# Kernel tuning notes

Measured on AMD Instinct MI355X. Metric: run time of the kernel, lower is better.

## Reference

```python
import jax, jax.numpy as jnp
import numpy as np

N_HEADS = 32
N_KV_HEADS = 8
HEAD_DIM = 128
DIM = 4096
BATCH = 2
SEQ = 2048


def rope_freqs(seqlen, head_dim, theta=10000.0):
    inv_freq = 1.0 / (theta ** (np.arange(0, head_dim, 2, dtype=np.float32) / head_dim))
    t = np.arange(seqlen, dtype=np.float32)
    ang = np.outer(t, inv_freq)  # [S, head_dim//2]
    return jnp.asarray(np.cos(ang)), jnp.asarray(np.sin(ang))


def setup_inputs() -> dict:
    key = jax.random.key(0)
    ks = jax.random.split(key, 5)
    x = jax.random.normal(ks[0], (BATCH, SEQ, DIM), dtype=jnp.float32)
    wq = jax.random.normal(ks[1], (N_HEADS * HEAD_DIM, DIM), dtype=jnp.float32) * 0.02
    wk = jax.random.normal(ks[2], (N_KV_HEADS * HEAD_DIM, DIM), dtype=jnp.float32) * 0.02
    wv = jax.random.normal(ks[3], (N_KV_HEADS * HEAD_DIM, DIM), dtype=jnp.float32) * 0.02
    wo = jax.random.normal(ks[4], (DIM, N_HEADS * HEAD_DIM), dtype=jnp.float32) * 0.02
    freqs_cos, freqs_sin = rope_freqs(SEQ, HEAD_DIM)
    return {"x": x, "freqs_cos": freqs_cos, "freqs_sin": freqs_sin,
            "wq": wq, "wk": wk, "wv": wv, "wo": wo}


def apply_rope(x, cos, sin):
    # x: [B, S, H, D]; complex multiply on consecutive pairs (even=real, odd=imag)
    xf = x.astype(jnp.float32).reshape(*x.shape[:-1], HEAD_DIM // 2, 2)
    x0, x1 = xf[..., 0], xf[..., 1]
    c = cos[None, :, None, :]  # [1, S, 1, D/2]
    s = sin[None, :, None, :]
    o0 = x0 * c - x1 * s
    o1 = x0 * s + x1 * c
    return jnp.stack([o0, o1], axis=-1).reshape(x.shape).astype(x.dtype)


def reference(x, freqs_cos, freqs_sin, wq, wk, wv, wo):
    b, s, _ = x.shape
    g = N_HEADS // N_KV_HEADS  # GQA group size
    xq = (x @ wq.T).reshape(b, s, N_HEADS, HEAD_DIM)
    xk = (x @ wk.T).reshape(b, s, N_KV_HEADS, HEAD_DIM)
    xv = (x @ wv.T).reshape(b, s, N_KV_HEADS, HEAD_DIM)
    xq = apply_rope(xq, freqs_cos, freqs_sin)
    xk = apply_rope(xk, freqs_cos, freqs_sin)
    # GQA: group query heads per kv head without repeating k/v
    q = xq.reshape(b, s, N_KV_HEADS, g, HEAD_DIM)
    scale = 1.0 / jnp.sqrt(jnp.asarray(HEAD_DIM, dtype=x.dtype))
    scores = jnp.einsum("bqkgd,bskd->bkgqs", q, xk) * scale  # [B, KV, G, S, S]
    causal = jnp.tril(jnp.ones((s, s), dtype=bool))
    scores = jnp.where(causal, scores, jnp.asarray(-jnp.inf, dtype=scores.dtype))
    probs = jax.nn.softmax(scores, axis=-1)
    out = jnp.einsum("bkgqs,bskd->bqkgd", probs, xv).reshape(b, s, N_HEADS * HEAD_DIM)
    return out @ wo.T
```

## Files before the change

### kernel.cpp

```cpp
#include <hip/hip_runtime.h>
#include <hip/hip_bf16.h>

typedef short short8_t __attribute__((ext_vector_type(8)));
typedef float float4_t __attribute__((ext_vector_type(4)));

#define MFMA16(A, B, C) __builtin_amdgcn_mfma_f32_16x16x32_bf16((A), (B), (C), 0, 0, 0)

#define SEQ 2048
#define HD 128
#define NH 32
#define NKV 8

__device__ inline short f2bs(float f) {
    union { __hip_bfloat16 h; short s; } u;
    u.h = __float2bfloat16(f);
    return u.s;
}

__device__ inline short8_t load8(const __hip_bfloat16* p) {
    return *(const short8_t*)p;
}
__device__ inline short8_t load8(const float* p) {
    float4_t a = *(const float4_t*)p;
    float4_t b = *(const float4_t*)(p + 4);
    short8_t r;
    r[0] = f2bs(a[0]); r[1] = f2bs(a[1]); r[2] = f2bs(a[2]); r[3] = f2bs(a[3]);
    r[4] = f2bs(b[0]); r[5] = f2bs(b[1]); r[6] = f2bs(b[2]); r[7] = f2bs(b[3]);
    return r;
}

__device__ inline void store_c(__hip_bfloat16* p, float v) { *p = __float2bfloat16(v); }
__device__ inline void store_c(float* p, float v)          { *p = v; }

__device__ __forceinline__ void gld_lds16(const __hip_bfloat16* g, __hip_bfloat16* l) {
    __builtin_amdgcn_global_load_lds(
        (const __attribute__((address_space(1))) unsigned int*)g,
        (__attribute__((address_space(3))) unsigned int*)l,
        16, 0, 0);
}

__global__ __launch_bounds__(256) void cvt_bf16(
    const float* __restrict__ in, __hip_bfloat16* __restrict__ out, int n8)
{
    int stride = gridDim.x * 256;
    for (int i = blockIdx.x * 256 + threadIdx.x; i < n8; i += stride) {
        short8_t r = load8(in + (size_t)i * 8);
        *(short8_t*)(out + (size_t)i * 8) = r;
    }
}

template <typename TC, bool TRC = false>
__global__ __launch_bounds__(256) void gemm_bt(
    const __hip_bfloat16* __restrict__ A,
    const __hip_bfloat16* __restrict__ B,
    TC* __restrict__ C,
    int M, int N, int K)
{
    __shared__ __hip_bfloat16 As[128 * 32];
    __shared__ __hip_bfloat16 Bs[128 * 32];

    const int tid  = threadIdx.x;
    const int wave = tid >> 6;
    const int lane = tid & 63;
    const int quad = lane >> 4;
    const int l16  = lane & 15;
    const int m0 = blockIdx.y * 128;
    const int n0 = blockIdx.x * 128;
    const int wm = (wave >> 1) * 64;
    const int wn = (wave & 1) * 64;

    const int row0 = tid >> 2;
    const int col0 = (tid & 3) * 8;

    const __hip_bfloat16* Abase = A + (size_t)m0 * K;
    const __hip_bfloat16* Bbase = B + (size_t)n0 * K;
    __hip_bfloat16* AsW = As + wave * 512;
    __hip_bfloat16* BsW = Bs + wave * 512;

    float4_t acc[4][4] = {};

    for (int k0 = 0; k0 < K; k0 += 32) {
        __syncthreads();
        gld_lds16(Abase + (size_t)row0        * K + k0 + col0, AsW);
        gld_lds16(Abase + (size_t)(row0 + 64) * K + k0 + col0, AsW + 2048);
        gld_lds16(Bbase + (size_t)row0        * K + k0 + col0, BsW);
        gld_lds16(Bbase + (size_t)(row0 + 64) * K + k0 + col0, BsW + 2048);
        __syncthreads();

        short8_t af[4], bf[4];
#pragma unroll
        for (int t = 0; t < 4; t++)
            af[t] = *(const short8_t*)&As[(wm + t * 16 + l16) * 32 + quad * 8];
#pragma unroll
        for (int t = 0; t < 4; t++)
            bf[t] = *(const short8_t*)&Bs[(wn + t * 16 + l16) * 32 + quad * 8];
#pragma unroll
        for (int mt = 0; mt < 4; mt++)
#pragma unroll
            for (int nt = 0; nt < 4; nt++)
                acc[mt][nt] = MFMA16(af[mt], bf[nt], acc[mt][nt]);
    }

#pragma unroll
    for (int mt = 0; mt < 4; mt++)
#pragma unroll
        for (int nt = 0; nt < 4; nt++)
#pragma unroll
            for (int r = 0; r < 4; r++) {
                int row = m0 + wm + mt * 16 + quad * 4 + r;
                int col = n0 + wn + nt * 16 + l16;
                if constexpr (TRC) {
                    int bb = row >> 11, ss = row & (SEQ - 1);
                    C[((size_t)bb * N + col) * SEQ + ss] = __float2bfloat16(acc[mt][nt][r]);
                } else {
                    store_c(&C[(size_t)row * N + col], acc[mt][nt][r]);
                }
            }
}

template <typename TC>
__global__ __launch_bounds__(512, 2) void gemm256(
    const __hip_bfloat16* __restrict__ A,
    const __hip_bfloat16* __restrict__ B,
    TC* __restrict__ C,
    int M, int N, int K)
{
    __shared__ __hip_bfloat16 lds[65536];
    __hip_bfloat16* ldsA0 = lds;
    __hip_bfloat16* ldsB0 = lds + 16384;
    __hip_bfloat16* ldsA1 = lds + 32768;
    __hip_bfloat16* ldsB1 = lds + 49152;

    const int tid  = threadIdx.x;
    const int wave = tid >> 6;
    const int lane = tid & 63;
    const int quad = lane >> 4;
    const int l16  = lane & 15;
    const int wm = wave >> 2;
    const int wn = wave & 3;
    const int m0 = blockIdx.y * 256;
    const int n0 = blockIdx.x * 256;

    const __hip_bfloat16* Abase = A + (size_t)m0 * K;
    const __hip_bfloat16* Bbase = B + (size_t)n0 * K;

    float4_t acc[8][4] = {};
    short8_t af[4][2], bf[2][2];

#define FENCE  asm volatile("" ::: "memory")
#define BAR    { FENCE; __builtin_amdgcn_s_barrier(); FENCE; }
#define LGKM0  { asm volatile("s_waitcnt lgkmcnt(0)" ::: "memory");          \
                 __builtin_amdgcn_sched_barrier(0); }
#define LGKM8  asm volatile("s_waitcnt lgkmcnt(8)" ::: "memory")
#define VM4    asm volatile("s_waitcnt vmcnt(4)" ::: "memory")
#define VM0    asm volatile("s_waitcnt vmcnt(0)" ::: "memory")

#define STAGE(GBASE, LTILE, T, H)                                            \
    {                                                                        \
        _Pragma("unroll")                                                    \
        for (int j = 0; j < 2; j++) {                                        \
            int c = j * 512 + tid;                                           \
            int r = c >> 3, s = c & 7;                                       \
            gld_lds16((GBASE) + (size_t)((H) * 128 + r) * K + (T) * 64 +     \
                          ((s ^ (r & 7)) * 8),                               \
                      (LTILE) + (H) * 8192 + j * 4096 + wave * 512);         \
        }                                                                    \
    }

#define LDA_(QM, ABASE)                                                      \
    {                                                                        \
        _Pragma("unroll")                                                    \
        for (int mt = 0; mt < 4; mt++)                                       \
            _Pragma("unroll")                                                \
            for (int kk = 0; kk < 2; kk++) {                                 \
                int row = (QM) * 128 + wm * 64 + mt * 16 + l16;              \
                int sc  = (kk * 4 + quad) ^ (row & 7);                       \
                af[mt][kk] = *(const short8_t*)&(ABASE)[row * 64 + sc * 8];  \
            }                                                                \
    }

#define LDB_(QN, BBASE)                                                      \
    {                                                                        \
        _Pragma("unroll")                                                    \
        for (int nt = 0; nt < 2; nt++)                                       \
            _Pragma("unroll")                                                \
            for (int kk = 0; kk < 2; kk++) {                                 \
                int row = (QN) * 128 + wn * 32 + nt * 16 + l16;              \
                int sc  = (kk * 4 + quad) ^ (row & 7);                       \
                bf[nt][kk] = *(const short8_t*)&(BBASE)[row * 64 + sc * 8];  \
            }                                                                \
    }

#define QMM(QM, QN)                                                          \
    __builtin_amdgcn_s_setprio(1);                                           \
    _Pragma("unroll")                                                        \
    for (int mt = 0; mt < 4; mt++)                                           \
        _Pragma("unroll")                                                    \
        for (int nt = 0; nt < 2; nt++)                                       \
            _Pragma("unroll")                                                \
            for (int kk = 0; kk < 2; kk++)                                   \
                acc[(QM) * 4 + mt][(QN) * 2 + nt] =                          \
                    MFMA16(af[mt][kk], bf[nt][kk],                           \
                           acc[(QM) * 4 + mt][(QN) * 2 + nt]);               \
    __builtin_amdgcn_s_setprio(0);

    STAGE(Abase, ldsA0, 0, 0);
    STAGE(Bbase, ldsB0, 0, 0);
    STAGE(Abase, ldsA0, 0, 1);
    STAGE(Bbase, ldsB0, 0, 1);
    STAGE(Abase, ldsA1, 1, 0);
    STAGE(Bbase, ldsB1, 1, 0);
    VM4;
    BAR;

    const int NIT = (K >> 7);
#pragma unroll 1
    for (int i = 0; i < NIT - 1; i++) {
        const int T0 = 2 * i, T1 = 2 * i + 1;
        LDA_(0, ldsA0); LDB_(0, ldsB0);
        STAGE(Bbase, ldsB1, T1, 1);
        LGKM8; BAR; LGKM0; QMM(0, 0); BAR;
        LDB_(1, ldsB0);
        STAGE(Abase, ldsA1, T1, 1);
        BAR; LGKM0; QMM(0, 1); BAR;
        LDA_(1, ldsA0); LDB_(0, ldsB0);
        STAGE(Abase, ldsA0, T0 + 2, 0);
        LGKM8; BAR; LGKM0; QMM(1, 0); BAR;
        LDB_(1, ldsB0);
        STAGE(Bbase, ldsB0, T0 + 2, 0);
        VM4; BAR; LGKM0; QMM(1, 1); BAR;
        LDA_(0, ldsA1); LDB_(0, ldsB1);
        STAGE(Bbase, ldsB0, T0 + 2, 1);
        LGKM8; BAR; LGKM0; QMM(0, 0); BAR;
        LDB_(1, ldsB1);
        STAGE(Abase, ldsA0, T0 + 2, 1);
        BAR; LGKM0; QMM(0, 1); BAR;
        LDA_(1, ldsA1); LDB_(0, ldsB1);
        STAGE(Abase, ldsA1, T1 + 2, 0);
        LGKM8; BAR; LGKM0; QMM(1, 0); BAR;
        LDB_(1, ldsB1);
        STAGE(Bbase, ldsB1, T1 + 2, 0);
        VM4; BAR; LGKM0; QMM(1, 1); BAR;
    }

    {
        const int TL = 2 * NIT - 1;
        LDA_(0, ldsA0); LDB_(0, ldsB0);
        STAGE(Bbase, ldsB1, TL, 1);
        LGKM8; BAR; LGKM0; QMM(0, 0); BAR;
        LDB_(1, ldsB0);
        STAGE(Abase, ldsA1, TL, 1);
        BAR; LGKM0; QMM(0, 1); BAR;
        LDA_(1, ldsA0); LDB_(0, ldsB0);
        LGKM8; BAR; LGKM0; QMM(1, 0); BAR;
        LDB_(1, ldsB0);
        VM0; BAR; LGKM0; QMM(1, 1); BAR;
        LDA_(0, ldsA1); LDB_(0, ldsB1); QMM(0, 0);
        LDB_(1, ldsB1);                 QMM(0, 1);
        LDA_(1, ldsA1); LDB_(0, ldsB1); QMM(1, 0);
        LDB_(1, ldsB1);                 QMM(1, 1);
    }

#pragma unroll
    for (int qm = 0; qm < 2; qm++)
#pragma unroll
        for (int mt = 0; mt < 4; mt++)
#pragma unroll
            for (int qn = 0; qn < 2; qn++)
#pragma unroll
                for (int nt = 0; nt < 2; nt++)
#pragma unroll
                    for (int r = 0; r < 4; r++) {
                        int row = m0 + qm * 128 + wm * 64 + mt * 16 + quad * 4 + r;
                        int col = n0 + qn * 128 + wn * 32 + nt * 16 + l16;
                        store_c(&C[(size_t)row * N + col], acc[qm * 4 + mt][qn * 2 + nt][r]);
                    }
#undef STAGE
#undef LDA_
#undef LDB_
#undef QMM
#undef FENCE
#undef BAR
#undef LGKM0
#undef LGKM8
#undef VM4
#undef VM0
}

__global__ __launch_bounds__(256) void rope_kernel(
    __hip_bfloat16* __restrict__ x,
    const float* __restrict__ cs,
    const float* __restrict__ sn,
    int npairs, int shift)
{
    int pi = blockIdx.x * 256 + threadIdx.x;
    if (pi >= npairs) return;
    int cols = 1 << shift;
    int cp   = pi & (cols - 1);
    int row  = pi >> shift;
    int d    = cp & 63;
    int pos  = row & (SEQ - 1);
    float c = cs[pos * 64 + d];
    float s = sn[pos * 64 + d];
    __hip_bfloat16* p = x + (((size_t)row) << (shift + 1)) + (size_t)cp * 2;
    float x0 = __bfloat162float(p[0]);
    float x1 = __bfloat162float(p[1]);
    p[0] = __float2bfloat16(x0 * c - x1 * s);
    p[1] = __float2bfloat16(x0 * s + x1 * c);
}

__global__ __launch_bounds__(512, 4) void flash_kernel(
    const __hip_bfloat16* __restrict__ Q,
    const __hip_bfloat16* __restrict__ Km,
    const __hip_bfloat16* __restrict__ VT,
    __hip_bfloat16* __restrict__ O)
{
    __shared__ __hip_bfloat16 smem[64 * 136 + 128 * 72];
    __hip_bfloat16* Ks = smem;
    __hip_bfloat16* Vt = smem + 64 * 136;

    const int tid  = threadIdx.x;
    const int wave = tid >> 6;
    const int lane = tid & 63;
    const int quad = lane >> 4;
    const int l16  = lane & 15;
    const int qt = ((int)blockIdx.x + (int)blockIdx.y + ((int)blockIdx.z << 4)) & 31;
    const int h  = (int)blockIdx.y * 2 + (wave >> 2);
    const int b  = blockIdx.z;
    const int kvh = blockIdx.y >> 1;
    const int q0  = qt * 64;
    const float scale = 0.08838834764831845f;
    const int qrow = q0 + (wave & 3) * 16 + l16;

    short8_t qf[4];
    {
        const __hip_bfloat16* qp = Q + (size_t)(b * SEQ + qrow) * (NH * HD) + h * HD + quad * 8;
#pragma unroll
        for (int kk = 0; kk < 4; kk++)
            qf[kk] = *(const short8_t*)(qp + kk * 32);
    }

    float4_t acc[8] = {};
    float m_st = -1e30f, l_st = 0.f;

    const __hip_bfloat16* vbase = VT + ((size_t)(b * NKV + kvh) * HD) * SEQ;
    const __hip_bfloat16* kbase = Km + (size_t)(b * SEQ) * (NKV * HD) + kvh * HD;

    const int krow0 = tid >> 4;
    const int kseg  = (tid & 15) * 8;
    const int vd0   = tid >> 3;
    const int vsl   = (tid & 7) * 8;

    uint4 kr0, kr1, vr0, vr1;
#define STAGE_LOAD(KT)                                                              \
    {                                                                               \
        kr0 = *(const uint4*)(kbase + (size_t)((KT) * 64 + krow0)      * (NKV * HD) + kseg); \
        kr1 = *(const uint4*)(kbase + (size_t)((KT) * 64 + krow0 + 32) * (NKV * HD) + kseg); \
        vr0 = *(const uint4*)(vbase + (size_t)vd0        * SEQ + (KT) * 64 + vsl);  \
        vr1 = *(const uint4*)(vbase + (size_t)(vd0 + 64) * SEQ + (KT) * 64 + vsl);  \
    }
#define STAGE_WRITE()                                         \
    {                                                         \
        *(uint4*)&Ks[(size_t)krow0        * 136 + kseg] = kr0; \
        *(uint4*)&Ks[(size_t)(krow0 + 32) * 136 + kseg] = kr1; \
        *(uint4*)&Vt[(size_t)vd0          * 72  + vsl]  = vr0; \
        *(uint4*)&Vt[(size_t)(vd0 + 64)   * 72  + vsl]  = vr1; \
    }

    STAGE_LOAD(0);
    STAGE_WRITE();
    __syncthreads();

    for (int kt = 0; kt <= qt; kt++) {
        const bool last = (kt == qt);
        if (!last) STAGE_LOAD(kt + 1);

        float4_t st[4] = {};
        __builtin_amdgcn_s_setprio(1);
#pragma unroll
        for (int kk = 0; kk < 4; kk++)
#pragma unroll
            for (int mt = 0; mt < 4; mt++) {
                short8_t kf = *(const short8_t*)&Ks[(size_t)(mt * 16 + l16) * 136 + kk * 32 + quad * 8];
                st[mt] = MFMA16(kf, qf[kk], st[mt]);
            }
        __builtin_amdgcn_s_setprio(0);

        float mx = -1e30f;
        if (last) {
#pragma unroll
            for (int mt = 0; mt < 4; mt++)
#pragma unroll
                for (int r = 0; r < 4; r++) {
                    int key = kt * 64 + mt * 16 + quad * 4 + r;
                    float s = st[mt][r] * scale;
                    if (key > qrow) s = -1e30f;
                    st[mt][r] = s;
                    mx = fmaxf(mx, s);
                }
        } else {
#pragma unroll
            for (int mt = 0; mt < 4; mt++)
#pragma unroll
                for (int r = 0; r < 4; r++) {
                    float s = st[mt][r] * scale;
                    st[mt][r] = s;
                    mx = fmaxf(mx, s);
                }
        }
        mx = fmaxf(mx, __shfl_xor(mx, 16, 64));
        mx = fmaxf(mx, __shfl_xor(mx, 32, 64));

        float mcur;
        if (__all(mx <= m_st + 8.f)) {
            mcur = m_st;
        } else {
            float mnew  = fmaxf(m_st, mx);
            float alpha = __expf(m_st - mnew);
            l_st *= alpha;
#pragma unroll
            for (int dm = 0; dm < 8; dm++)
                acc[dm] *= alpha;
            m_st = mnew;
            mcur = mnew;
        }

        uint32_t pk[4][2];
        float rsum = 0.f;
#pragma unroll
        for (int mt = 0; mt < 4; mt++)
#pragma unroll
            for (int hh = 0; hh < 2; hh++) {
                float p0 = __expf(st[mt][2 * hh]     - mcur);
                float p1 = __expf(st[mt][2 * hh + 1] - mcur);
                rsum += p0 + p1;
                pk[mt][hh] = (uint32_t)(unsigned short)f2bs(p0) |
                             ((uint32_t)(unsigned short)f2bs(p1) << 16);
            }
        rsum += __shfl_xor(rsum, 16, 64);
        rsum += __shfl_xor(rsum, 32, 64);
        l_st += rsum;

        const int src0 = ((quad & 1) * 2) * 16 + l16;
        const int src1 = src0 + 16;
        const bool hi_mt = (quad >> 1) != 0;
#pragma unroll
        for (int kk2 = 0; kk2 < 2; kk2++) {
            uint32_t a0 = (uint32_t)__shfl((int)pk[kk2 * 2][0],     src0, 64);
            uint32_t a1 = (uint32_t)__shfl((int)pk[kk2 * 2][1],     src0, 64);
            uint32_t a2 = (uint32_t)__shfl((int)pk[kk2 * 2][0],     src1, 64);
            uint32_t a3 = (uint32_t)__shfl((int)pk[kk2 * 2][1],     src1, 64);
            uint32_t b0 = (uint32_t)__shfl((int)pk[kk2 * 2 + 1][0], src0, 64);
            uint32_t b1 = (uint32_t)__shfl((int)pk[kk2 * 2 + 1][1], src0, 64);
            uint32_t b2 = (uint32_t)__shfl((int)pk[kk2 * 2 + 1][0], src1, 64);
            uint32_t b3 = (uint32_t)__shfl((int)pk[kk2 * 2 + 1][1], src1, 64);
            union { uint32_t u[4]; short8_t v; } pf;
            pf.u[0] = hi_mt ? b0 : a0;
            pf.u[1] = hi_mt ? b1 : a1;
            pf.u[2] = hi_mt ? b2 : a2;
            pf.u[3] = hi_mt ? b3 : a3;
            __builtin_amdgcn_s_setprio(1);
#pragma unroll
            for (int dm = 0; dm < 8; dm++) {
                short8_t vf = *(const short8_t*)&Vt[(size_t)(dm * 16 + l16) * 72 + kk2 * 32 + quad * 8];
                acc[dm] = MFMA16(vf, pf.v, acc[dm]);
            }
            __builtin_amdgcn_s_setprio(0);
        }

        __syncthreads();
        if (!last) {
            STAGE_WRITE();
            __syncthreads();
        }
    }

    __hip_bfloat16* Ot = smem;
    float inv_l = 1.f / l_st;
#pragma unroll
    for (int dm = 0; dm < 8; dm++)
#pragma unroll
        for (int hh = 0; hh < 2; hh++) {
            uint32_t pv = (uint32_t)(unsigned short)f2bs(acc[dm][2 * hh] * inv_l) |
                          ((uint32_t)(unsigned short)f2bs(acc[dm][2 * hh + 1] * inv_l) << 16);
            *(uint32_t*)&Ot[(size_t)(wave * 16 + l16) * 136 + dm * 16 + quad * 4 + 2 * hh] = pv;
        }
    __syncthreads();
#pragma unroll
    for (int i = 0; i < 4; i++) {
        int c  = i * 64 + lane;
        int r2 = c >> 4, ch = c & 15;
        uint4 v = *(const uint4*)&Ot[(size_t)(wave * 16 + r2) * 136 + ch * 8];
        *(uint4*)(O + (size_t)(b * SEQ + q0 + (wave & 3) * 16 + r2) * (NH * HD) + h * HD + ch * 8) = v;
    }
#undef STAGE_LOAD
#undef STAGE_WRITE
}

extern "C" void kernel_launch(void* const* d_in, const int* in_sizes, int n_in,
                              void* d_out, int out_size, void* d_ws, size_t ws_size,
                              hipStream_t stream)
{
    const float* x  = (const float*)d_in[0];
    const float* fc = (const float*)d_in[1];
    const float* fs = (const float*)d_in[2];
    const float* wq = (const float*)d_in[3];
    const float* wk = (const float*)d_in[4];
    const float* wv = (const float*)d_in[5];
    const float* wo = (const float*)d_in[6];
    float* out = (float*)d_out;

    const int BS = 2 * SEQ;
    char* ws = (char*)d_ws;
    __hip_bfloat16* q    = (__hip_bfloat16*)(ws);
    __hip_bfloat16* k    = (__hip_bfloat16*)(ws + 33554432ull);
    __hip_bfloat16* vT   = (__hip_bfloat16*)(ws + 41943040ull);
    __hip_bfloat16* xb   = (__hip_bfloat16*)(ws + 50331648ull);
    __hip_bfloat16* attn = xb;
    __hip_bfloat16* wb   = (__hip_bfloat16*)(ws + 83886080ull);

    cvt_bf16<<<2048, 256, 0, stream>>>(x,  xb, (BS * 4096) / 8);
    cvt_bf16<<<2048, 256, 0, stream>>>(wq, wb, (4096 * 4096) / 8);
    gemm256<__hip_bfloat16><<<dim3(16, 16), 512, 0, stream>>>(xb, wb, q, BS, NH * HD, 4096);
    cvt_bf16<<<2048, 256, 0, stream>>>(wk, wb, (1024 * 4096) / 8);
    gemm_bt<__hip_bfloat16, false><<<dim3(8, 32), 256, 0, stream>>>(xb, wb, k, BS, NKV * HD, 4096);
    cvt_bf16<<<2048, 256, 0, stream>>>(wv, wb, (1024 * 4096) / 8);
    gemm_bt<__hip_bfloat16, true ><<<dim3(8, 32), 256, 0, stream>>>(xb, wb, vT, BS, NKV * HD, 4096);

    {
        int npq = BS * NH * 64;
        rope_kernel<<<(npq + 255) / 256, 256, 0, stream>>>(q, fc, fs, npq, 11);
        int npk = BS * NKV * 64;
        rope_kernel<<<(npk + 255) / 256, 256, 0, stream>>>(k, fc, fs, npk, 9);
    }

    flash_kernel<<<dim3(SEQ / 64, NH / 2, 2), 512, 0, stream>>>(q, k, vT, attn);

    cvt_bf16<<<2048, 256, 0, stream>>>(wo, wb, (4096 * 4096) / 8);
    gemm256<float><<<dim3(16, 16), 512, 0, stream>>>(attn, wb, out, BS, NH * HD, 4096);
}
```

Baseline: 806.3 us.

## Fuse K and V projections into one GEMM and XOR-swizzle flash LDS tiles

Converts wk and wv into adjacent bf16 buffers and runs one combined GEMM that writes K row-major and V transposed, replacing two smaller launches with a single wider grid. In the flash kernel, the padded LDS layouts for K, V^T and the output staging tile are replaced by unpadded rows with an XOR swizzle, to avoid bank conflicts while using less shared memory. The combined GEMM adds a per-element branch in its epilogue, and the swizzle has to be matched exactly between the writes and the reads.

Measured after the change: 745.3 us. 7.6% less time.

```diff
diff --git a/kernel.cpp b/kernel.cpp
--- a/kernel.cpp
+++ b/kernel.cpp
@@ -49,12 +49,12 @@
     }
 }
 
-template <typename TC, bool TRC = false>
-__global__ __launch_bounds__(256) void gemm_bt(
+__global__ __launch_bounds__(256) void gemm_kv(
     const __hip_bfloat16* __restrict__ A,
     const __hip_bfloat16* __restrict__ B,
-    TC* __restrict__ C,
-    int M, int N, int K)
+    __hip_bfloat16* __restrict__ Kout,
+    __hip_bfloat16* __restrict__ VTout,
+    int M, int K)
 {
     __shared__ __hip_bfloat16 As[128 * 32];
     __shared__ __hip_bfloat16 Bs[128 * 32];
@@ -109,11 +109,12 @@
             for (int r = 0; r < 4; r++) {
                 int row = m0 + wm + mt * 16 + quad * 4 + r;
                 int col = n0 + wn + nt * 16 + l16;
-                if constexpr (TRC) {
+                __hip_bfloat16 v = __float2bfloat16(acc[mt][nt][r]);
+                if (col < 1024) {
+                    Kout[(size_t)row * 1024 + col] = v;
+                } else {
                     int bb = row >> 11, ss = row & (SEQ - 1);
-                    C[((size_t)bb * N + col) * SEQ + ss] = __float2bfloat16(acc[mt][nt][r]);
-                } else {
-                    store_c(&C[(size_t)row * N + col], acc[mt][nt][r]);
+                    VTout[((size_t)bb * 1024 + (col - 1024)) * SEQ + ss] = v;
                 }
             }
 }
@@ -315,9 +316,9 @@
     const __hip_bfloat16* __restrict__ VT,
     __hip_bfloat16* __restrict__ O)
 {
-    __shared__ __hip_bfloat16 smem[64 * 136 + 128 * 72];
-    __hip_bfloat16* Ks = smem;
-    __hip_bfloat16* Vt = smem + 64 * 136;
+    __shared__ __hip_bfloat16 smem[16384];
+    char* KsB = (char*)smem;
+    char* VtB = (char*)smem + 16384;
 
     const int tid  = threadIdx.x;
     const int wave = tid >> 6;
@@ -331,6 +332,7 @@
     const int q0  = qt * 64;
     const float scale = 0.08838834764831845f;
     const int qrow = q0 + (wave & 3) * 16 + l16;
+    const int xk = (l16 & 7) << 4;
 
     short8_t qf[4];
     {
@@ -350,6 +352,10 @@
     const int kseg  = (tid & 15) * 8;
     const int vd0   = tid >> 3;
     const int vsl   = (tid & 7) * 8;
+    const int wK0 = krow0 * 256 + ((kseg * 2) ^ ((krow0 & 7) << 4));
+    const int wK1 = wK0 + 32 * 256;
+    const int wV0 = vd0 * 128 + ((vsl * 2) ^ ((vd0 & 7) << 4));
+    const int wV1 = wV0 + 64 * 128;
 
     uint4 kr0, kr1, vr0, vr1;
 #define STAGE_LOAD(KT)                                                              \
@@ -359,12 +365,12 @@
         vr0 = *(const uint4*)(vbase + (size_t)vd0        * SEQ + (KT) * 64 + vsl);  \
         vr1 = *(const uint4*)(vbase + (size_t)(vd0 + 64) * SEQ + (KT) * 64 + vsl);  \
     }
-#define STAGE_WRITE()                                         \
-    {                                                         \
-        *(uint4*)&Ks[(size_t)krow0        * 136 + kseg] = kr0; \
-        *(uint4*)&Ks[(size_t)(krow0 + 32) * 136 + kseg] = kr1; \
-        *(uint4*)&Vt[(size_t)vd0          * 72  + vsl]  = vr0; \
-        *(uint4*)&Vt[(size_t)(vd0 + 64)   * 72  + vsl]  = vr1; \
+#define STAGE_WRITE()                          \
+    {                                          \
+        *(uint4*)(KsB + wK0) = kr0;            \
+        *(uint4*)(KsB + wK1) = kr1;            \
+        *(uint4*)(VtB + wV0) = vr0;            \
+        *(uint4*)(VtB + wV1) = vr1;            \
     }
 
     STAGE_LOAD(0);
@@ -381,7 +387,8 @@
         for (int kk = 0; kk < 4; kk++)
 #pragma unroll
             for (int mt = 0; mt < 4; mt++) {
-                short8_t kf = *(const short8_t*)&Ks[(size_t)(mt * 16 + l16) * 136 + kk * 32 + quad * 8];
+                short8_t kf = *(const short8_t*)(KsB + (mt * 16 + l16) * 256 +
+                                                 ((kk * 64 + quad * 16) ^ xk));
                 st[mt] = MFMA16(kf, qf[kk], st[mt]);
             }
         __builtin_amdgcn_s_setprio(0);
@@ -462,7 +469,8 @@
             __builtin_amdgcn_s_setprio(1);
 #pragma unroll
             for (int dm = 0; dm < 8; dm++) {
-                short8_t vf = *(const short8_t*)&Vt[(size_t)(dm * 16 + l16) * 72 + kk2 * 32 + quad * 8];
+                short8_t vf = *(const short8_t*)(VtB + (dm * 16 + l16) * 128 +
+                                                 ((kk2 * 64 + quad * 16) ^ xk));
                 acc[dm] = MFMA16(vf, pf.v, acc[dm]);
             }
             __builtin_amdgcn_s_setprio(0);
@@ -475,7 +483,7 @@
         }
     }
 
-    __hip_bfloat16* Ot = smem;
+    char* OtB = (char*)smem;
     float inv_l = 1.f / l_st;
 #pragma unroll
     for (int dm = 0; dm < 8; dm++)
@@ -483,14 +491,16 @@
         for (int hh = 0; hh < 2; hh++) {
             uint32_t pv = (uint32_t)(unsigned short)f2bs(acc[dm][2 * hh] * inv_l) |
                           ((uint32_t)(unsigned short)f2bs(acc[dm][2 * hh + 1] * inv_l) << 16);
-            *(uint32_t*)&Ot[(size_t)(wave * 16 + l16) * 136 + dm * 16 + quad * 4 + 2 * hh] = pv;
+            *(uint32_t*)(OtB + (wave * 16 + l16) * 256 +
+                         ((dm * 32 + quad * 8 + 4 * hh) ^ xk)) = pv;
         }
     __syncthreads();
 #pragma unroll
     for (int i = 0; i < 4; i++) {
         int c  = i * 64 + lane;
         int r2 = c >> 4, ch = c & 15;
-        uint4 v = *(const uint4*)&Ot[(size_t)(wave * 16 + r2) * 136 + ch * 8];
+        uint4 v = *(const uint4*)(OtB + (wave * 16 + r2) * 256 +
+                                  ((ch * 16) ^ ((r2 & 7) << 4)));
         *(uint4*)(O + (size_t)(b * SEQ + q0 + (wave & 3) * 16 + r2) * (NH * HD) + h * HD + ch * 8) = v;
     }
 #undef STAGE_LOAD
@@ -522,10 +532,10 @@
     cvt_bf16<<<2048, 256, 0, stream>>>(x,  xb, (BS * 4096) / 8);
     cvt_bf16<<<2048, 256, 0, stream>>>(wq, wb, (4096 * 4096) / 8);
     gemm256<__hip_bfloat16><<<dim3(16, 16), 512, 0, stream>>>(xb, wb, q, BS, NH * HD, 4096);
-    cvt_bf16<<<2048, 256, 0, stream>>>(wk, wb, (1024 * 4096) / 8);
-    gemm_bt<__hip_bfloat16, false><<<dim3(8, 32), 256, 0, stream>>>(xb, wb, k, BS, NKV * HD, 4096);
-    cvt_bf16<<<2048, 256, 0, stream>>>(wv, wb, (1024 * 4096) / 8);
-    gemm_bt<__hip_bfloat16, true ><<<dim3(8, 32), 256, 0, stream>>>(xb, wb, vT, BS, NKV * HD, 4096);
+
+    cvt_bf16<<<2048, 256, 0, stream>>>(wk, wb,                 (1024 * 4096) / 8);
+    cvt_bf16<<<2048, 256, 0, stream>>>(wv, wb + 4194304ull,    (1024 * 4096) / 8);
+    gemm_kv<<<dim3(16, 32), 256, 0, stream>>>(xb, wb, k, vT, BS, 4096);
 
     {
         int npq = BS * NH * 64;
```
